# Optimization experiments

Hardware: AMD Instinct MI355X
Metric: run time of the kernel (lower is better)

Reference implementation:

```python
import jax, jax.numpy as jnp
import numpy as np

B, N, V, E, T = 32, 256, 16, 1024, 5
MAX_N, ANNO, ND, VD, A_ACT = 256, 18, 64, 64, 3


def position_encoding_init(n_position, emb_dim):
    pe = np.array([[pos / np.power(10000, 2 * (j // 2) / emb_dim) for j in range(emb_dim)]
                   if pos != 0 else np.zeros(emb_dim) for pos in range(n_position)])
    pe[1:, 0::2] = np.sin(pe[1:, 0::2])
    pe[1:, 1::2] = np.cos(pe[1:, 1::2])
    return jnp.asarray(pe, jnp.float32)


def gru_cell(x, h, Wih, Whh, bih=None, bhh=None):
    # PyTorch GRUCell semantics. Wih: [3H, in], Whh: [3H, H]
    gi = x @ Wih.T + (bih if bih is not None else 0.0)
    gh = h @ Whh.T + (bhh if bhh is not None else 0.0)
    i_r, i_z, i_n = jnp.split(gi, 3, axis=1)
    h_r, h_z, h_n = jnp.split(gh, 3, axis=1)
    r = jax.nn.sigmoid(i_r + h_r)
    z = jax.nn.sigmoid(i_z + h_z)
    n = jnp.tanh(i_n + r * h_n)
    return (1.0 - z) * n + z * h


def setup_inputs() -> dict:
    key = jax.random.key(0)
    ks = jax.random.split(key, 20)
    dec_in = E + ND + 2 * VD
    inp = {
        "annotation": jax.random.normal(ks[0], (B, N, ANNO), jnp.float32),
        "A_out": jax.random.bernoulli(ks[1], 0.05, (B, N, N)).astype(jnp.float32),
        "A_in": jax.random.bernoulli(ks[2], 0.05, (B, N, N)).astype(jnp.float32),
        "from_node": jax.random.randint(ks[3], (B,), 0, MAX_N),
        "vnf_now": jax.random.uniform(ks[4], (B, V), jnp.float32),
        "vnf_all": jax.random.uniform(ks[5], (B, V), jnp.float32),
        "mask": jax.random.randint(ks[6], (B * N,), 0, 2),
        "anno_W": jax.random.normal(ks[7], (ANNO, E), jnp.float32),
        "gru_Wih": jax.random.normal(ks[8], (3 * E, 2 * E), jnp.float32) / np.sqrt(2 * E),
        "gru_Whh": jax.random.normal(ks[9], (3 * E, E), jnp.float32) / np.sqrt(E),
        "vnf_now_W": jax.random.normal(ks[10], (V, VD), jnp.float32),
        "vnf_all_W": jax.random.normal(ks[11], (V, VD), jnp.float32),
        "dgru_Wih": jax.random.normal(ks[12], (6 * E, dec_in), jnp.float32) / np.sqrt(dec_in),
        "dgru_Whh": jax.random.normal(ks[13], (6 * E, 2 * E), jnp.float32) / np.sqrt(2 * E),
        "dgru_bih": jax.random.normal(ks[14], (6 * E,), jnp.float32) * 0.01,
        "dgru_bhh": jax.random.normal(ks[15], (6 * E,), jnp.float32) * 0.01,
        "out_W1": jax.random.normal(ks[16], (E, 2 * E), jnp.float32) / np.sqrt(2 * E),
        "out_b1": jnp.zeros((E,), jnp.float32),
        "out_W2": jax.random.normal(ks[17], (A_ACT, E), jnp.float32) / np.sqrt(E),
        "out_b2": jnp.zeros((A_ACT,), jnp.float32),
        "pos_enc": position_encoding_init(MAX_N, ND),
    }
    return inp


def reference(annotation, A_out, A_in, from_node, vnf_now, vnf_all, mask,
              anno_W, gru_Wih, gru_Whh, vnf_now_W, vnf_all_W,
              dgru_Wih, dgru_Whh, dgru_bih, dgru_bhh,
              out_W1, out_b1, out_W2, out_b2, pos_enc):
    BN = B * N
    # ---- encoder (GG-NN): block-diagonal adjacency matmul == batched matmul ----
    h = annotation.reshape(BN, ANNO) @ anno_W  # [BN, E]

    def step(h, _):
        hb = h.reshape(B, N, E)
        a_out = jnp.einsum('bnm,bme->bne', A_out, hb).reshape(BN, E)
        a_in = jnp.einsum('bnm,bme->bne', A_in, hb).reshape(BN, E)
        a = jnp.concatenate([a_out, a_in], axis=1)  # [BN, 2E]
        return gru_cell(a, h, gru_Wih, gru_Whh), None

    enc_out, _ = jax.lax.scan(step, h, None, length=T)  # [BN, E]

    # ---- decoder step ----
    vn = (vnf_now @ vnf_now_W)[:, None, :]  # [B,1,VD] (repeat over N)
    va = (vnf_all @ vnf_all_W)[:, None, :]
    npos = pos_enc[from_node][:, None, :]   # [B,1,ND]
    vn = jnp.broadcast_to(vn, (B, N, VD)).reshape(BN, VD)
    va = jnp.broadcast_to(va, (B, N, VD)).reshape(BN, VD)
    npos = jnp.broadcast_to(npos, (B, N, ND)).reshape(BN, ND)

    concat_input = jnp.concatenate([enc_out, npos, va, vn], axis=1)
    h0 = jnp.zeros((BN, 2 * E), jnp.float32)
    hidden = gru_cell(concat_input, h0, dgru_Wih, dgru_Whh, dgru_bih, dgru_bhh)

    mid = jax.nn.relu(hidden @ out_W1.T + out_b1)
    output = (mid @ out_W2.T + out_b2).reshape(B, N, A_ACT)

    max_v = jnp.max(output, axis=(1, 2), keepdims=True)  # [B,1,1]
    output = output - (max_v + 1.0)
    mask_f = jnp.where(mask == 1, 1.0, 1e10).astype(jnp.float32).reshape(B, N, 1)
    output = mask_f * output + 1.0

    node_logits = output[:, :, 0]            # [B, N]
    vnf_logits = output[:, :, 1:]            # [B, N, 2]
    return node_logits, vnf_logits, hidden
```

## Files before the change

kernel.cpp:

```cpp
#include <hip/hip_runtime.h>
#include <hip/hip_bf16.h>
#include <math.h>

#define B_ 32
#define N_ 256
#define E_ 1024
#define BN_ 8192

typedef __hip_bfloat16 bf16;
typedef __bf16 bf8v __attribute__((ext_vector_type(8)));
typedef float  f4v  __attribute__((ext_vector_type(4)));

__device__ __forceinline__ float b2f(bf16 v) {
    unsigned short u = *(unsigned short*)&v;
    return __uint_as_float(((unsigned)u) << 16);
}
__device__ __forceinline__ unsigned short f2bu(float f) {
    bf16 h = __float2bfloat16(f);
    return *(unsigned short*)&h;
}
__device__ __forceinline__ float4 load4bf(const bf16* p) {
    ushort4 u = *(const ushort4*)p;
    return make_float4(__uint_as_float((unsigned)u.x << 16),
                       __uint_as_float((unsigned)u.y << 16),
                       __uint_as_float((unsigned)u.z << 16),
                       __uint_as_float((unsigned)u.w << 16));
}
__device__ __forceinline__ void store4bf(bf16* p, float a, float b, float c, float d) {
    ushort4 u = make_ushort4(f2bu(a), f2bu(b), f2bu(c), f2bu(d));
    *(ushort4*)p = u;
}
__device__ __forceinline__ float safe_sigm(float x) {
    x = fminf(fmaxf(x, -40.0f), 40.0f);
    return 1.0f / (1.0f + expf(-x));
}
__device__ __forceinline__ float safe_tanh(float x) {
    x = fminf(fmaxf(x, -15.0f), 15.0f);
    float t = expf(2.0f * x);
    return (t - 1.0f) / (t + 1.0f);
}
__device__ __forceinline__ void glds16(const bf16* g, bf16* l) {
    __builtin_amdgcn_global_load_lds(
        (__attribute__((address_space(1))) const void*)g,
        (__attribute__((address_space(3))) void*)l, 16, 0, 0);
}

#define MFMA16(d, a, b) d = __builtin_amdgcn_mfma_f32_16x16x32_bf16(a, b, d, 0, 0, 0)

__global__ __launch_bounds__(256)
void w2bf_kernel(const float* __restrict__ src, bf16* __restrict__ dst, int n4)
{
    int i = blockIdx.x * 256 + threadIdx.x;
    if (i < n4) {
        float4 v = ((const float4*)src)[i];
        store4bf(dst + (size_t)i * 4, v.x, v.y, v.z, v.w);
    }
}

__global__ __launch_bounds__(256)
void wgpack_kernel(const float* __restrict__ Wih, const float* __restrict__ Whh,
                   bf16* __restrict__ Wg)
{
    const int wr = blockIdx.x;
    const int e16 = wr / 48, rem = wr % 48;
    const int gate = rem >> 4, eL = rem & 15;
    const int e = e16 * 16 + eL;
    const float* s1 = Wih + (size_t)(gate * 1024 + e) * 2048;
    const float* s2 = Whh + (size_t)(gate * 1024 + e) * 1024;
    bf16* d = Wg + (size_t)wr * 3072;
    const int k0 = threadIdx.x * 4;
#pragma unroll
    for (int rep = 0; rep < 2; ++rep) {
        int k = k0 + rep * 1024;
        float4 v = *(const float4*)(s1 + k);
        store4bf(d + k, v.x, v.y, v.z, v.w);
    }
    {
        float4 v = *(const float4*)(s2 + k0);
        store4bf(d + 2048 + k0, v.x, v.y, v.z, v.w);
    }
}

__global__ __launch_bounds__(256)
void dgpack_kernel(const float* __restrict__ Wih, bf16* __restrict__ Wg)
{
    const int wr = blockIdx.x;
    const int e16 = wr / 48, rem = wr % 48;
    const int gate = rem >> 4, eL = rem & 15;
    const int e = e16 * 16 + eL;
    const float* s = Wih + (size_t)(gate * 2048 + e) * 1216;
    bf16* d = Wg + (size_t)wr * 1216;
    for (int k4 = threadIdx.x; k4 < 304; k4 += 256) {
        float4 v = *(const float4*)(s + k4 * 4);
        store4bf(d + k4 * 4, v.x, v.y, v.z, v.w);
    }
}

__global__ __launch_bounds__(256)
void anno_kernel(const float* __restrict__ anno, const float* __restrict__ W,
                 float* __restrict__ H)
{
    __shared__ float s[18];
    int row = blockIdx.x;
    if (threadIdx.x < 18) s[threadIdx.x] = anno[row * 18 + threadIdx.x];
    __syncthreads();
    for (int j = threadIdx.x; j < 1024; j += 256) {
        float acc = 0.0f;
#pragma unroll
        for (int k = 0; k < 18; ++k) acc = fmaf(s[k], W[k * 1024 + j], acc);
        H[(size_t)row * 1024 + j] = acc;
    }
}

__global__ __launch_bounds__(256)
void bmm_kernel(const float* __restrict__ Aout, const float* __restrict__ Ain,
                const float* __restrict__ H, bf16* __restrict__ Abuf)
{
    __shared__ float As[16][68];
    __shared__ float Bs[16][68];
    const int z = blockIdx.z;
    const int b = z >> 1, which = z & 1;
    const float* Amat = (which ? Ain : Aout) + (size_t)b * N_ * N_;
    const float* Bmat = H + (size_t)b * N_ * E_;
    const int t = threadIdx.x;
    const int tx = t & 15, ty = t >> 4;
    const int bm = blockIdx.x * 64;
    const int bn = blockIdx.y * 64;
    const int ar = t >> 2, ak = (t & 3) << 2;
    const int kr = t >> 4, kn = (t & 15) << 2;
    float acc[4][4] = {};
    for (int k0 = 0; k0 < N_; k0 += 16) {
        float4 av = *(const float4*)(Amat + (size_t)(bm + ar) * N_ + k0 + ak);
        As[ak + 0][ar] = av.x; As[ak + 1][ar] = av.y;
        As[ak + 2][ar] = av.z; As[ak + 3][ar] = av.w;
        float4 bv = *(const float4*)(Bmat + (size_t)(k0 + kr) * E_ + bn + kn);
        *(float4*)&Bs[kr][kn] = bv;
        __syncthreads();
#pragma unroll
        for (int kk = 0; kk < 16; ++kk) {
            float4 a4 = *(const float4*)&As[kk][ty << 2];
            float4 b4 = *(const float4*)&Bs[kk][tx << 2];
            float am[4] = {a4.x, a4.y, a4.z, a4.w};
            float bb[4] = {b4.x, b4.y, b4.z, b4.w};
#pragma unroll
            for (int i = 0; i < 4; ++i)
#pragma unroll
                for (int j = 0; j < 4; ++j)
                    acc[i][j] = fmaf(am[i], bb[j], acc[i][j]);
        }
        __syncthreads();
    }
#pragma unroll
    for (int i = 0; i < 4; ++i) {
        int row = b * N_ + bm + (ty << 2) + i;
        int col = which * 1024 + bn + (tx << 2);
        store4bf(&Abuf[(size_t)row * 2048 + col], acc[i][0], acc[i][1], acc[i][2], acc[i][3]);
    }
}

__global__ __launch_bounds__(256)
void htrans_kernel(const float* __restrict__ H, bf16* __restrict__ HbT)
{
    __shared__ float s[64][65];
    const int b = blockIdx.z;
    const int e0 = blockIdx.x * 64;
    const int n0 = blockIdx.y * 64;
    const float* Hb = H + (size_t)b * N_ * E_;
    bf16* Tb = HbT + (size_t)b * E_ * N_;
    const int t = threadIdx.x;
    const int tr = t >> 4, tc = (t & 15) << 2;
#pragma unroll
    for (int i = 0; i < 4; ++i) {
        float4 v = *(const float4*)(Hb + (size_t)(n0 + tr + i * 16) * E_ + e0 + tc);
        s[tr + i * 16][tc + 0] = v.x; s[tr + i * 16][tc + 1] = v.y;
        s[tr + i * 16][tc + 2] = v.z; s[tr + i * 16][tc + 3] = v.w;
    }
    __syncthreads();
#pragma unroll
    for (int i = 0; i < 4; ++i) {
        int e = tr + i * 16;
        store4bf(Tb + (size_t)(e0 + e) * N_ + n0 + tc,
                 s[tc + 0][e], s[tc + 1][e], s[tc + 2][e], s[tc + 3][e]);
    }
}

__global__ __launch_bounds__(256)
void bmm_mfma_kernel(const bf16* __restrict__ Aoutb, const bf16* __restrict__ Ainb,
                     const bf16* __restrict__ HbT, bf16* __restrict__ Abuf)
{
    __shared__ bf16 As[64 * 32];
    __shared__ bf16 Bs[64 * 32];
    const int t = threadIdx.x;
    const int lane = t & 63, w = t >> 6;
    const int wm = (w >> 1) * 32, wn = (w & 1) * 32;
    const int z = blockIdx.z, b = z >> 1, which = z & 1;
    const int bm = blockIdx.x * 64, bn = blockIdx.y * 64;
    const int quad = lane >> 4, fr = lane & 15;
    const int srow = t >> 2, slot = t & 3;
    const int g = (slot + ((srow >> 1) & 3)) & 3;
    const int lds_off = srow * 32 + slot * 8;

    f4v acc[2][2];
#pragma unroll
    for (int i = 0; i < 2; ++i)
#pragma unroll
        for (int j = 0; j < 2; ++j) acc[i][j] = (f4v){0.f, 0.f, 0.f, 0.f};

    int aoff[2], boff[2];
#pragma unroll
    for (int i = 0; i < 2; ++i) {
        int arow = wm + 16 * i + fr;
        int s = (quad - ((arow >> 1) & 3)) & 3;
        aoff[i] = arow * 32 + s * 8;
    }
#pragma unroll
    for (int j = 0; j < 2; ++j) {
        int n = wn + 16 * j + fr;
        int s = (quad - ((n >> 1) & 3)) & 3;
        boff[j] = n * 32 + s * 8;
    }

    const bf16* Ap = (which ? Ainb : Aoutb) + (size_t)b * N_ * N_
                   + (size_t)(bm + srow) * N_ + g * 8;
    const bf16* Bp = HbT + (size_t)b * E_ * N_ + (size_t)(bn + srow) * N_ + g * 8;
    for (int k0 = 0; k0 < N_; k0 += 32) {
        float4 av = *(const float4*)(Ap + k0);
        float4 bv4 = *(const float4*)(Bp + k0);
        __syncthreads();
        *(float4*)(As + lds_off) = av;
        *(float4*)(Bs + lds_off) = bv4;
        __syncthreads();
        bf8v af0 = *(const bf8v*)(As + aoff[0]);
        bf8v af1 = *(const bf8v*)(As + aoff[1]);
#pragma unroll
        for (int j = 0; j < 2; ++j) {
            bf8v bv = *(const bf8v*)(Bs + boff[j]);
            MFMA16(acc[0][j], af0, bv);
            MFMA16(acc[1][j], af1, bv);
        }
    }
#pragma unroll
    for (int i = 0; i < 2; ++i)
#pragma unroll
        for (int j = 0; j < 2; ++j)
#pragma unroll
            for (int r = 0; r < 4; ++r) {
                int row = b * N_ + bm + wm + 16 * i + quad * 4 + r;
                int col = which * 1024 + bn + wn + 16 * j + fr;
                Abuf[(size_t)row * 2048 + col] = __float2bfloat16(acc[i][j][r]);
            }
}

__global__ __launch_bounds__(256, 2)
void enc_gru_kernel(const bf16* __restrict__ Aab, const bf16* __restrict__ Wg,
                    const float* __restrict__ Hcur, float* __restrict__ Hnext)
{
    __shared__ __align__(16) bf16 As[2 * 128 * 32];
    __shared__ __align__(16) bf16 Bs[2 * 192 * 32];
    const int t = threadIdx.x;
    const int lane = t & 63, w = t >> 6;
    const int wm = (w >> 1) * 64;
    const int wnH = (w & 1);
    const int bm = blockIdx.x * 128;
    const int bY = blockIdx.y;
    const int quad = lane >> 4, fr = lane & 15;

    f4v ar[2][4], az[2][4], ani[2][4], anh[2][4];
#pragma unroll
    for (int gq = 0; gq < 2; ++gq)
#pragma unroll
        for (int i = 0; i < 4; ++i) {
            ar[gq][i] = (f4v){0.f, 0.f, 0.f, 0.f};
            az[gq][i] = (f4v){0.f, 0.f, 0.f, 0.f};
            ani[gq][i] = (f4v){0.f, 0.f, 0.f, 0.f};
            anh[gq][i] = (f4v){0.f, 0.f, 0.f, 0.f};
        }

    int aoff[4];
#pragma unroll
    for (int i = 0; i < 4; ++i) {
        int row = wm + 16 * i + fr;
        int s = (quad - ((row >> 1) & 3)) & 3;
        aoff[i] = row * 32 + s * 8;
    }
    int boff[2][3];
#pragma unroll
    for (int gq = 0; gq < 2; ++gq)
#pragma unroll
        for (int gt = 0; gt < 3; ++gt) {
            int nb = wnH * 96 + gq * 48 + gt * 16 + fr;
            int s = (quad - ((nb >> 1) & 3)) & 3;
            boff[gq][gt] = nb * 32 + s * 8;
        }

    const int sr = lane >> 2, ss = lane & 3;
    const int lrA0 = w * 16 + sr;
    const int lrA1 = 64 + w * 16 + sr;
    const int gA0 = (ss + ((lrA0 >> 1) & 3)) & 3;
    const int gA1 = (ss + ((lrA1 >> 1) & 3)) & 3;
    const bf16* apA0 = Aab + (size_t)(bm + lrA0) * 2048 + gA0 * 8;
    const bf16* apA1 = Aab + (size_t)(bm + lrA1) * 2048 + gA1 * 8;
    const int lrB0 = w * 16 + sr, lrB1 = 64 + w * 16 + sr, lrB2 = 128 + w * 16 + sr;
    const int gB0 = (ss + ((lrB0 >> 1) & 3)) & 3;
    const int gB1 = (ss + ((lrB1 >> 1) & 3)) & 3;
    const int gB2 = (ss + ((lrB2 >> 1) & 3)) & 3;
    const bf16* bp0 = Wg + (size_t)(bY * 192 + lrB0) * 3072 + gB0 * 8;
    const bf16* bp1 = Wg + (size_t)(bY * 192 + lrB1) * 3072 + gB1 * 8;
    const bf16* bp2 = Wg + (size_t)(bY * 192 + lrB2) * 3072 + gB2 * 8;
    const int oA0 = (w * 16) * 32, oA1 = (64 + w * 16) * 32;
    const int oB0 = (w * 16) * 32, oB1 = (64 + w * 16) * 32, oB2 = (128 + w * 16) * 32;

#define ENC_STEP(Ab, Bb, AN) do {                                              \
    bf8v af0 = *(const bf8v*)((Ab) + aoff[0]);                                 \
    bf8v af1 = *(const bf8v*)((Ab) + aoff[1]);                                 \
    bf8v af2 = *(const bf8v*)((Ab) + aoff[2]);                                 \
    bf8v af3 = *(const bf8v*)((Ab) + aoff[3]);                                 \
    _Pragma("unroll")                                                          \
    for (int gq = 0; gq < 2; ++gq) {                                           \
        bf8v br_ = *(const bf8v*)((Bb) + boff[gq][0]);                         \
        bf8v bz_ = *(const bf8v*)((Bb) + boff[gq][1]);                         \
        bf8v bn_ = *(const bf8v*)((Bb) + boff[gq][2]);                         \
        MFMA16(ar[gq][0], af0, br_); MFMA16(ar[gq][1], af1, br_);              \
        MFMA16(ar[gq][2], af2, br_); MFMA16(ar[gq][3], af3, br_);              \
        MFMA16(az[gq][0], af0, bz_); MFMA16(az[gq][1], af1, bz_);              \
        MFMA16(az[gq][2], af2, bz_); MFMA16(az[gq][3], af3, bz_);              \
        MFMA16(AN[gq][0], af0, bn_); MFMA16(AN[gq][1], af1, bn_);              \
        MFMA16(AN[gq][2], af2, bn_); MFMA16(AN[gq][3], af3, bn_);              \
    }                                                                          \
} while (0)

    glds16(apA0, As + oA0);
    glds16(apA1, As + oA1);
    glds16(bp0, Bs + oB0);
    glds16(bp1, Bs + oB1);
    glds16(bp2, Bs + oB2);
    __syncthreads();
    int cur = 0;
    for (int k0 = 0; k0 < 2048; k0 += 32) {
        const int nb = cur ^ 1;
        if (k0 + 32 < 2048) {
            glds16(apA0 + k0 + 32, As + nb * 4096 + oA0);
            glds16(apA1 + k0 + 32, As + nb * 4096 + oA1);
            glds16(bp0 + k0 + 32, Bs + nb * 6144 + oB0);
            glds16(bp1 + k0 + 32, Bs + nb * 6144 + oB1);
            glds16(bp2 + k0 + 32, Bs + nb * 6144 + oB2);
        }
        const bf16* Ab = As + cur * 4096;
        const bf16* Bb = Bs + cur * 6144;
        ENC_STEP(Ab, Bb, ani);
        __syncthreads();
        cur = nb;
    }

    {
        const int tr = t >> 1;
        const int c0 = (t & 1) * 2;
        const int rr_ = (tr >> 1) & 3;
        const int s0 = (c0 - rr_) & 3;
        const int s1 = (c0 + 1 - rr_) & 3;
        const float* hp = Hcur + (size_t)(bm + tr) * 1024 + c0 * 8;
        for (int k0 = 2048; k0 < 3072; k0 += 32) {
            const int k2 = k0 - 2048;
            float4 f0 = *(const float4*)(hp + k2);
            float4 f1 = *(const float4*)(hp + k2 + 4);
            float4 f2 = *(const float4*)(hp + k2 + 8);
            float4 f3 = *(const float4*)(hp + k2 + 12);
            uint4 u0, u1;
            u0.x = (unsigned)f2bu(f0.x) | ((unsigned)f2bu(f0.y) << 16);
            u0.y = (unsigned)f2bu(f0.z) | ((unsigned)f2bu(f0.w) << 16);
            u0.z = (unsigned)f2bu(f1.x) | ((unsigned)f2bu(f1.y) << 16);
            u0.w = (unsigned)f2bu(f1.z) | ((unsigned)f2bu(f1.w) << 16);
            u1.x = (unsigned)f2bu(f2.x) | ((unsigned)f2bu(f2.y) << 16);
            u1.y = (unsigned)f2bu(f2.z) | ((unsigned)f2bu(f2.w) << 16);
            u1.z = (unsigned)f2bu(f3.x) | ((unsigned)f2bu(f3.y) << 16);
            u1.w = (unsigned)f2bu(f3.z) | ((unsigned)f2bu(f3.w) << 16);
            __syncthreads();
            *(uint4*)(As + tr * 32 + s0 * 8) = u0;
            *(uint4*)(As + tr * 32 + s1 * 8) = u1;
            glds16(bp0 + k0, Bs + oB0);
            glds16(bp1 + k0, Bs + oB1);
            glds16(bp2 + k0, Bs + oB2);
            __syncthreads();
            ENC_STEP(As, Bs, anh);
        }
    }

#pragma unroll
    for (int gq = 0; gq < 2; ++gq) {
        const int e = bY * 64 + wnH * 32 + gq * 16 + fr;
#pragma unroll
        for (int i = 0; i < 4; ++i) {
#pragma unroll
            for (int r = 0; r < 4; ++r) {
                const int row = bm + wm + 16 * i + quad * 4 + r;
                float hv = Hcur[(size_t)row * 1024 + e];
                float rg = safe_sigm(ar[gq][i][r]);
                float zg = safe_sigm(az[gq][i][r]);
                float ng = safe_tanh(ani[gq][i][r] + rg * anh[gq][i][r]);
                Hnext[(size_t)row * 1024 + e] = (1.0f - zg) * ng + zg * hv;
            }
        }
    }
#undef ENC_STEP
}

__global__ __launch_bounds__(256, 2)
void dec_gru_kernel(const bf16* __restrict__ Cc, const bf16* __restrict__ Wg,
                    const float* __restrict__ bih, const float* __restrict__ bhh,
                    float* __restrict__ hidden)
{
    __shared__ __align__(16) bf16 As[2 * 128 * 32];
    __shared__ __align__(16) bf16 Bs[2 * 192 * 32];
    const int t = threadIdx.x;
    const int lane = t & 63, w = t >> 6;
    const int wm = (w >> 1) * 64;
    const int wnH = (w & 1);
    const int bm = blockIdx.x * 128;
    const int bY = blockIdx.y;
    const int quad = lane >> 4, fr = lane & 15;

    f4v ag[3][2][4];
#pragma unroll
    for (int c = 0; c < 3; ++c)
#pragma unroll
        for (int gq = 0; gq < 2; ++gq)
#pragma unroll
            for (int i = 0; i < 4; ++i) ag[c][gq][i] = (f4v){0.f, 0.f, 0.f, 0.f};

    int aoff[4];
#pragma unroll
    for (int i = 0; i < 4; ++i) {
        int row = wm + 16 * i + fr;
        int s = (quad - ((row >> 1) & 3)) & 3;
        aoff[i] = row * 32 + s * 8;
    }
    int boff[2][3];
#pragma unroll
    for (int gq = 0; gq < 2; ++gq)
#pragma unroll
        for (int gt = 0; gt < 3; ++gt) {
            int nb = wnH * 96 + gq * 48 + gt * 16 + fr;
            int s = (quad - ((nb >> 1) & 3)) & 3;
            boff[gq][gt] = nb * 32 + s * 8;
        }

    const int sr = lane >> 2, ss = lane & 3;
    const int lrA0 = w * 16 + sr;
    const int lrA1 = 64 + w * 16 + sr;
    const int gA0 = (ss + ((lrA0 >> 1) & 3)) & 3;
    const int gA1 = (ss + ((lrA1 >> 1) & 3)) & 3;
    const bf16* apA0 = Cc + (size_t)(bm + lrA0) * 1216 + gA0 * 8;
    const bf16* apA1 = Cc + (size_t)(bm + lrA1) * 1216 + gA1 * 8;
    const int lrB0 = w * 16 + sr, lrB1 = 64 + w * 16 + sr, lrB2 = 128 + w * 16 + sr;
    const int gB0 = (ss + ((lrB0 >> 1) & 3)) & 3;
    const int gB1 = (ss + ((lrB1 >> 1) & 3)) & 3;
    const int gB2 = (ss + ((lrB2 >> 1) & 3)) & 3;
    const bf16* bp0 = Wg + (size_t)(bY * 192 + lrB0) * 1216 + gB0 * 8;
    const bf16* bp1 = Wg + (size_t)(bY * 192 + lrB1) * 1216 + gB1 * 8;
    const bf16* bp2 = Wg + (size_t)(bY * 192 + lrB2) * 1216 + gB2 * 8;
    const int oA0 = (w * 16) * 32, oA1 = (64 + w * 16) * 32;
    const int oB0 = (w * 16) * 32, oB1 = (64 + w * 16) * 32, oB2 = (128 + w * 16) * 32;

    glds16(apA0, As + oA0);
    glds16(apA1, As + oA1);
    glds16(bp0, Bs + oB0);
    glds16(bp1, Bs + oB1);
    glds16(bp2, Bs + oB2);
    __syncthreads();
    int cur = 0;
    for (int k0 = 0; k0 < 1216; k0 += 32) {
        const int nb = cur ^ 1;
        if (k0 + 32 < 1216) {
            glds16(apA0 + k0 + 32, As + nb * 4096 + oA0);
            glds16(apA1 + k0 + 32, As + nb * 4096 + oA1);
            glds16(bp0 + k0 + 32, Bs + nb * 6144 + oB0);
            glds16(bp1 + k0 + 32, Bs + nb * 6144 + oB1);
            glds16(bp2 + k0 + 32, Bs + nb * 6144 + oB2);
        }
        const bf16* Ab = As + cur * 4096;
        const bf16* Bb = Bs + cur * 6144;
        bf8v af0 = *(const bf8v*)(Ab + aoff[0]);
        bf8v af1 = *(const bf8v*)(Ab + aoff[1]);
        bf8v af2 = *(const bf8v*)(Ab + aoff[2]);
        bf8v af3 = *(const bf8v*)(Ab + aoff[3]);
#pragma unroll
        for (int gq = 0; gq < 2; ++gq) {
            bf8v br_ = *(const bf8v*)(Bb + boff[gq][0]);
            bf8v bz_ = *(const bf8v*)(Bb + boff[gq][1]);
            bf8v bn_ = *(const bf8v*)(Bb + boff[gq][2]);
            MFMA16(ag[0][gq][0], af0, br_); MFMA16(ag[0][gq][1], af1, br_);
            MFMA16(ag[0][gq][2], af2, br_); MFMA16(ag[0][gq][3], af3, br_);
            MFMA16(ag[1][gq][0], af0, bz_); MFMA16(ag[1][gq][1], af1, bz_);
            MFMA16(ag[1][gq][2], af2, bz_); MFMA16(ag[1][gq][3], af3, bz_);
            MFMA16(ag[2][gq][0], af0, bn_); MFMA16(ag[2][gq][1], af1, bn_);
            MFMA16(ag[2][gq][2], af2, bn_); MFMA16(ag[2][gq][3], af3, bn_);
        }
        __syncthreads();
        cur = nb;
    }

#pragma unroll
    for (int gq = 0; gq < 2; ++gq) {
        const int e = bY * 64 + wnH * 32 + gq * 16 + fr;
        const float br = bih[e] + bhh[e];
        const float bz = bih[2048 + e] + bhh[2048 + e];
        const float bni = bih[4096 + e];
        const float bnh = bhh[4096 + e];
#pragma unroll
        for (int i = 0; i < 4; ++i) {
#pragma unroll
            for (int r = 0; r < 4; ++r) {
                const int row = bm + wm + 16 * i + quad * 4 + r;
                float rr = safe_sigm(ag[0][gq][i][r] + br);
                float zz = safe_sigm(ag[1][gq][i][r] + bz);
                float nn = safe_tanh(ag[2][gq][i][r] + bni + rr * bnh);
                hidden[(size_t)row * 2048 + e] = (1.0f - zz) * nn;
            }
        }
    }
}

__global__ __launch_bounds__(128)
void vnva_kernel(const float* __restrict__ vnf_now, const float* __restrict__ vnf_all,
                 const float* __restrict__ Wn, const float* __restrict__ Wa,
                 float* __restrict__ vn, float* __restrict__ va)
{
    int b = blockIdx.x, t = threadIdx.x;
    if (t < 64) {
        float s = 0.f;
#pragma unroll
        for (int k = 0; k < 16; ++k) s = fmaf(vnf_now[b * 16 + k], Wn[k * 64 + t], s);
        vn[b * 64 + t] = s;
    } else {
        int d = t - 64;
        float s = 0.f;
#pragma unroll
        for (int k = 0; k < 16; ++k) s = fmaf(vnf_all[b * 16 + k], Wa[k * 64 + d], s);
        va[b * 64 + d] = s;
    }
}

__global__ __launch_bounds__(256)
void concat_kernel(const float* __restrict__ H, const float* __restrict__ pos_enc,
                   const int* __restrict__ from_node, const float* __restrict__ va,
                   const float* __restrict__ vn, bf16* __restrict__ Cc)
{
    int row = blockIdx.x;
    int b = row >> 8;
    int fn = from_node[b];
    bf16* dst = Cc + (size_t)row * 1216;
    for (int c = threadIdx.x; c < 1216; c += 256) {
        float v;
        if (c < 1024)      v = H[(size_t)row * 1024 + c];
        else if (c < 1088) v = pos_enc[fn * 64 + (c - 1024)];
        else if (c < 1152) v = va[b * 64 + (c - 1088)];
        else               v = vn[b * 64 + (c - 1152)];
        dst[c] = __float2bfloat16(v);
    }
}

__global__ __launch_bounds__(256)
void out1_mfma_kernel(const float* __restrict__ H, const bf16* __restrict__ W1b,
                      const float* __restrict__ bias, bf16* __restrict__ mid)
{
    __shared__ bf16 As[64 * 32];
    __shared__ bf16 Ws[256 * 32];
    const int t = threadIdx.x;
    const int lane = t & 63, w = t >> 6;
    const int bm = blockIdx.x * 64, bn = blockIdx.y * 256;
    const int quad = lane >> 4, fr = lane & 15;
    const int srow = t >> 2, slot = t & 3;
    const int g = (slot + ((srow >> 1) & 3)) & 3;
    const int lds_off = srow * 32 + slot * 8;

    f4v acc[4][4];
#pragma unroll
    for (int i = 0; i < 4; ++i)
#pragma unroll
        for (int j = 0; j < 4; ++j) acc[i][j] = (f4v){0.f, 0.f, 0.f, 0.f};

    int aoff[4], boff[4];
#pragma unroll
    for (int i = 0; i < 4; ++i) {
        int arow = 16 * i + fr;
        int s = (quad - ((arow >> 1) & 3)) & 3;
        aoff[i] = arow * 32 + s * 8;
    }
#pragma unroll
    for (int j = 0; j < 4; ++j) {
        int n = w * 64 + 16 * j + fr;
        int s = (quad - ((n >> 1) & 3)) & 3;
        boff[j] = n * 32 + s * 8;
    }

    const float* Hp = H + (size_t)(bm + srow) * 2048 + g * 8;
    const bf16* Wp0 = W1b + (size_t)(bn + srow) * 2048 + g * 8;
    const bf16* Wp1 = W1b + (size_t)(bn + srow + 64) * 2048 + g * 8;
    const bf16* Wp2 = W1b + (size_t)(bn + srow + 128) * 2048 + g * 8;
    const bf16* Wp3 = W1b + (size_t)(bn + srow + 192) * 2048 + g * 8;

    for (int k0 = 0; k0 < 2048; k0 += 32) {
        float4 h0 = *(const float4*)(Hp + k0);
        float4 h1 = *(const float4*)(Hp + k0 + 4);
        float4 w0 = *(const float4*)(Wp0 + k0);
        float4 w1 = *(const float4*)(Wp1 + k0);
        float4 w2 = *(const float4*)(Wp2 + k0);
        float4 w3 = *(const float4*)(Wp3 + k0);
        uint4 pk;
        pk.x = (unsigned)f2bu(h0.x) | ((unsigned)f2bu(h0.y) << 16);
        pk.y = (unsigned)f2bu(h0.z) | ((unsigned)f2bu(h0.w) << 16);
        pk.z = (unsigned)f2bu(h1.x) | ((unsigned)f2bu(h1.y) << 16);
        pk.w = (unsigned)f2bu(h1.z) | ((unsigned)f2bu(h1.w) << 16);
        __syncthreads();
        *(uint4*)(As + lds_off) = pk;
        *(float4*)(Ws + lds_off) = w0;
        *(float4*)(Ws + 2048 + lds_off) = w1;
        *(float4*)(Ws + 4096 + lds_off) = w2;
        *(float4*)(Ws + 6144 + lds_off) = w3;
        __syncthreads();
        bf8v af0 = *(const bf8v*)(As + aoff[0]);
        bf8v af1 = *(const bf8v*)(As + aoff[1]);
        bf8v af2 = *(const bf8v*)(As + aoff[2]);
        bf8v af3 = *(const bf8v*)(As + aoff[3]);
#pragma unroll
        for (int j = 0; j < 4; ++j) {
            bf8v bv = *(const bf8v*)(Ws + boff[j]);
            MFMA16(acc[0][j], af0, bv);
            MFMA16(acc[1][j], af1, bv);
            MFMA16(acc[2][j], af2, bv);
            MFMA16(acc[3][j], af3, bv);
        }
    }
#pragma unroll
    for (int j = 0; j < 4; ++j) {
        const int col = bn + w * 64 + 16 * j + fr;
        const float bb = bias[col];
#pragma unroll
        for (int i = 0; i < 4; ++i) {
#pragma unroll
            for (int r = 0; r < 4; ++r) {
                const int row = bm + 16 * i + quad * 4 + r;
                mid[(size_t)row * 1024 + col] = __float2bfloat16(fmaxf(acc[i][j][r] + bb, 0.0f));
            }
        }
    }
}

__global__ __launch_bounds__(64)
void out2_kernel(const bf16* __restrict__ mid, const float* __restrict__ W2,
                 const float* __restrict__ b2, float* __restrict__ outb)
{
    int row = blockIdx.x, t = threadIdx.x;
    float s0 = 0.f, s1 = 0.f, s2 = 0.f;
    for (int k = t; k < 1024; k += 64) {
        float m = b2f(mid[(size_t)row * 1024 + k]);
        s0 = fmaf(m, W2[k], s0);
        s1 = fmaf(m, W2[1024 + k], s1);
        s2 = fmaf(m, W2[2048 + k], s2);
    }
#pragma unroll
    for (int off = 32; off > 0; off >>= 1) {
        s0 += __shfl_down(s0, off, 64);
        s1 += __shfl_down(s1, off, 64);
        s2 += __shfl_down(s2, off, 64);
    }
    if (t == 0) {
        outb[row * 3 + 0] = s0 + b2[0];
        outb[row * 3 + 1] = s1 + b2[1];
        outb[row * 3 + 2] = s2 + b2[2];
    }
}

__global__ __launch_bounds__(64)
void max_kernel(const float* __restrict__ outb, float* __restrict__ maxb)
{
    int b = blockIdx.x, t = threadIdx.x;
    float m = -3.0e38f;
    for (int i = t; i < 768; i += 64) m = fmaxf(m, outb[b * 768 + i]);
#pragma unroll
    for (int off = 32; off > 0; off >>= 1) m = fmaxf(m, __shfl_down(m, off, 64));
    if (t == 0) maxb[b] = m;
}

__global__ __launch_bounds__(256)
void mask_kernel(const float* __restrict__ outb, const float* __restrict__ maxb,
                 const int* __restrict__ mask, float* __restrict__ out)
{
    int idx = blockIdx.x * 256 + threadIdx.x;
    if (idx >= BN_ * 3) return;
    int row = idx / 3, c = idx - row * 3;
    int b = row >> 8;
    float v = outb[idx] - (maxb[b] + 1.0f);
    float mf = (mask[row] == 1) ? 1.0f : 1e10f;
    v = mf * v + 1.0f;
    if (c == 0) out[row] = v;
    else        out[8192 + row * 2 + (c - 1)] = v;
}

extern "C" void kernel_launch(void* const* d_in, const int* in_sizes, int n_in,
                              void* d_out, int out_size, void* d_ws, size_t ws_size,
                              hipStream_t stream)
{
    const float* annotation = (const float*)d_in[0];
    const float* A_out      = (const float*)d_in[1];
    const float* A_in       = (const float*)d_in[2];
    const int*   from_node  = (const int*)d_in[3];
    const float* vnf_now    = (const float*)d_in[4];
    const float* vnf_all    = (const float*)d_in[5];
    const int*   mask       = (const int*)d_in[6];
    const float* anno_W     = (const float*)d_in[7];
    const float* gru_Wih    = (const float*)d_in[8];
    const float* gru_Whh    = (const float*)d_in[9];
    const float* vnf_now_W  = (const float*)d_in[10];
    const float* vnf_all_W  = (const float*)d_in[11];
    const float* dgru_Wih   = (const float*)d_in[12];
    const float* dgru_bih   = (const float*)d_in[14];
    const float* dgru_bhh   = (const float*)d_in[15];
    const float* out_W1     = (const float*)d_in[16];
    const float* out_b1     = (const float*)d_in[17];
    const float* out_W2     = (const float*)d_in[18];
    const float* out_b2     = (const float*)d_in[19];
    const float* pos_enc    = (const float*)d_in[20];
    float* out = (float*)d_out;

    bf16*  Abuf = (bf16*)d_ws;
    bf16*  Wenc = Abuf + (size_t)8192 * 2048;
    bf16*  Wg   = Wenc;
    bf16*  WgD  = Wenc;
    bf16*  W1b  = Wenc;
    float* fbuf = (float*)(Wenc + (size_t)9437184);
    float* vnb  = fbuf;
    float* vab  = vnb + 2048;
    float* outb = vab + 2048;
    float* maxb = outb + 24576;
    bf16*  Aoutb = (bf16*)(maxb + 32);
    bf16*  Ainb  = Aoutb + (size_t)32 * 256 * 256;
    bf16*  HbT   = Ainb + (size_t)32 * 256 * 256;

    const size_t NEED_FULL = (size_t)(16777216 + 9437184) * 2 + 28704 * 4
                           + (size_t)(4194304 + 8388608) * 2;
    const bool full = ws_size >= NEED_FULL;

    float* hidden = out + 24576;
    float* H0 = hidden;
    float* H1 = H0 + (size_t)8192 * 1024;
    bf16* Cc  = Abuf;
    bf16* mid = Abuf;

    wgpack_kernel<<<3072, 256, 0, stream>>>(gru_Wih, gru_Whh, Wg);
    if (full) {
        w2bf_kernel<<<2048, 256, 0, stream>>>(A_out, Aoutb, 32 * 256 * 256 / 4);
        w2bf_kernel<<<2048, 256, 0, stream>>>(A_in,  Ainb,  32 * 256 * 256 / 4);
    }

    anno_kernel<<<8192, 256, 0, stream>>>(annotation, anno_W, H0);

    const float* hc = H0;
    float* hn = H1;
    for (int s = 0; s < 5; ++s) {
        if (full) {
            htrans_kernel<<<dim3(16, 4, 32), 256, 0, stream>>>(hc, HbT);
            bmm_mfma_kernel<<<dim3(4, 16, 64), 256, 0, stream>>>(Aoutb, Ainb, HbT, Abuf);
        } else {
            bmm_kernel<<<dim3(4, 16, 64), 256, 0, stream>>>(A_out, A_in, hc, Abuf);
        }
        enc_gru_kernel<<<dim3(64, 16), 256, 0, stream>>>(Abuf, Wg, hc, hn);
        float* tmp = (float*)hc; hc = hn; hn = tmp;
    }

    vnva_kernel<<<32, 128, 0, stream>>>(vnf_now, vnf_all, vnf_now_W, vnf_all_W, vnb, vab);
    concat_kernel<<<8192, 256, 0, stream>>>(hc, pos_enc, from_node, vab, vnb, Cc);

    dgpack_kernel<<<6144, 256, 0, stream>>>(dgru_Wih, WgD);
    dec_gru_kernel<<<dim3(64, 32), 256, 0, stream>>>(Cc, WgD, dgru_bih, dgru_bhh, hidden);

    w2bf_kernel<<<2048, 256, 0, stream>>>(out_W1, W1b, 1024 * 2048 / 4);
    out1_mfma_kernel<<<dim3(128, 4), 256, 0, stream>>>(hidden, W1b, out_b1, mid);

    out2_kernel<<<8192, 64, 0, stream>>>(mid, out_W2, out_b2, outb);
    max_kernel<<<32, 64, 0, stream>>>(outb, maxb);
    mask_kernel<<<96, 256, 0, stream>>>(outb, maxb, mask, out);
}
```

Baseline: 1.668 ms.

## Store encoder hidden state in bf16 and pipeline GRU K-loop with async staging

The encoder hidden state H moves from fp32 to bf16 storage throughout: anno, htrans, bmm, enc_gru and concat. This halves hidden-state traffic and lets the Hcur part of the GRU GEMM be staged with async global-to-LDS loads instead of converting on the fly with extra barriers. The GRU K-loop becomes a deeper software pipeline that keeps two stages in flight, using explicit vmcnt waits and raw barriers. The risk is extra rounding error from carrying the recurrent state in bf16 across the five steps.

```diff
diff --git a/kernel.cpp b/kernel.cpp
--- a/kernel.cpp
+++ b/kernel.cpp
@@ -98,7 +98,7 @@
 
 __global__ __launch_bounds__(256)
 void anno_kernel(const float* __restrict__ anno, const float* __restrict__ W,
-                 float* __restrict__ H)
+                 bf16* __restrict__ Hb)
 {
     __shared__ float s[18];
     int row = blockIdx.x;
@@ -108,20 +108,20 @@
         float acc = 0.0f;
 #pragma unroll
         for (int k = 0; k < 18; ++k) acc = fmaf(s[k], W[k * 1024 + j], acc);
-        H[(size_t)row * 1024 + j] = acc;
+        Hb[(size_t)row * 1024 + j] = __float2bfloat16(acc);
     }
 }
 
 __global__ __launch_bounds__(256)
 void bmm_kernel(const float* __restrict__ Aout, const float* __restrict__ Ain,
-                const float* __restrict__ H, bf16* __restrict__ Abuf)
+                const bf16* __restrict__ H, bf16* __restrict__ Abuf)
 {
     __shared__ float As[16][68];
     __shared__ float Bs[16][68];
     const int z = blockIdx.z;
     const int b = z >> 1, which = z & 1;
     const float* Amat = (which ? Ain : Aout) + (size_t)b * N_ * N_;
-    const float* Bmat = H + (size_t)b * N_ * E_;
+    const bf16* Bmat = H + (size_t)b * N_ * E_;
     const int t = threadIdx.x;
     const int tx = t & 15, ty = t >> 4;
     const int bm = blockIdx.x * 64;
@@ -133,7 +133,7 @@
         float4 av = *(const float4*)(Amat + (size_t)(bm + ar) * N_ + k0 + ak);
         As[ak + 0][ar] = av.x; As[ak + 1][ar] = av.y;
         As[ak + 2][ar] = av.z; As[ak + 3][ar] = av.w;
-        float4 bv = *(const float4*)(Bmat + (size_t)(k0 + kr) * E_ + bn + kn);
+        float4 bv = load4bf(Bmat + (size_t)(k0 + kr) * E_ + bn + kn);
         *(float4*)&Bs[kr][kn] = bv;
         __syncthreads();
 #pragma unroll
@@ -159,19 +159,19 @@
 }
 
 __global__ __launch_bounds__(256)
-void htrans_kernel(const float* __restrict__ H, bf16* __restrict__ HbT)
+void htrans_kernel(const bf16* __restrict__ H, bf16* __restrict__ HbT)
 {
     __shared__ float s[64][65];
     const int b = blockIdx.z;
     const int e0 = blockIdx.x * 64;
     const int n0 = blockIdx.y * 64;
-    const float* Hb = H + (size_t)b * N_ * E_;
+    const bf16* Hb = H + (size_t)b * N_ * E_;
     bf16* Tb = HbT + (size_t)b * E_ * N_;
     const int t = threadIdx.x;
     const int tr = t >> 4, tc = (t & 15) << 2;
 #pragma unroll
     for (int i = 0; i < 4; ++i) {
-        float4 v = *(const float4*)(Hb + (size_t)(n0 + tr + i * 16) * E_ + e0 + tc);
+        float4 v = load4bf(Hb + (size_t)(n0 + tr + i * 16) * E_ + e0 + tc);
         s[tr + i * 16][tc + 0] = v.x; s[tr + i * 16][tc + 1] = v.y;
         s[tr + i * 16][tc + 2] = v.z; s[tr + i * 16][tc + 3] = v.w;
     }
@@ -253,7 +253,7 @@
 
 __global__ __launch_bounds__(256, 2)
 void enc_gru_kernel(const bf16* __restrict__ Aab, const bf16* __restrict__ Wg,
-                    const float* __restrict__ Hcur, float* __restrict__ Hnext)
+                    const bf16* __restrict__ Hcur, bf16* __restrict__ Hnext)
 {
     __shared__ __align__(16) bf16 As[2 * 128 * 32];
     __shared__ __align__(16) bf16 Bs[2 * 192 * 32];
@@ -300,6 +300,8 @@
     const int gA1 = (ss + ((lrA1 >> 1) & 3)) & 3;
     const bf16* apA0 = Aab + (size_t)(bm + lrA0) * 2048 + gA0 * 8;
     const bf16* apA1 = Aab + (size_t)(bm + lrA1) * 2048 + gA1 * 8;
+    const bf16* hpA0 = Hcur + (size_t)(bm + lrA0) * 1024 + gA0 * 8;
+    const bf16* hpA1 = Hcur + (size_t)(bm + lrA1) * 1024 + gA1 * 8;
     const int lrB0 = w * 16 + sr, lrB1 = 64 + w * 16 + sr, lrB2 = 128 + w * 16 + sr;
     const int gB0 = (ss + ((lrB0 >> 1) & 3)) & 3;
     const int gB1 = (ss + ((lrB1 >> 1) & 3)) & 3;
@@ -309,6 +311,17 @@
     const bf16* bp2 = Wg + (size_t)(bY * 192 + lrB2) * 3072 + gB2 * 8;
     const int oA0 = (w * 16) * 32, oA1 = (64 + w * 16) * 32;
     const int oB0 = (w * 16) * 32, oB1 = (64 + w * 16) * 32, oB2 = (128 + w * 16) * 32;
+
+#define ENC_STAGE(K, BUF) do {                                                 \
+    const int k_ = (K);                                                        \
+    const bf16* a0_ = (k_ < 2048) ? apA0 + k_ : hpA0 + (k_ - 2048);            \
+    const bf16* a1_ = (k_ < 2048) ? apA1 + k_ : hpA1 + (k_ - 2048);            \
+    glds16(a0_, As + (BUF) * 4096 + oA0);                                      \
+    glds16(a1_, As + (BUF) * 4096 + oA1);                                      \
+    glds16(bp0 + k_, Bs + (BUF) * 6144 + oB0);                                 \
+    glds16(bp1 + k_, Bs + (BUF) * 6144 + oB1);                                 \
+    glds16(bp2 + k_, Bs + (BUF) * 6144 + oB2);                                 \
+} while (0)
 
 #define ENC_STEP(Ab, Bb, AN) do {                                              \
     bf8v af0 = *(const bf8v*)((Ab) + aoff[0]);                                 \
@@ -329,61 +342,30 @@
     }                                                                          \
 } while (0)
 
-    glds16(apA0, As + oA0);
-    glds16(apA1, As + oA1);
-    glds16(bp0, Bs + oB0);
-    glds16(bp1, Bs + oB1);
-    glds16(bp2, Bs + oB2);
-    __syncthreads();
+    ENC_STAGE(0, 0);
+    ENC_STAGE(32, 1);
     int cur = 0;
+#pragma unroll 2
     for (int k0 = 0; k0 < 2048; k0 += 32) {
-        const int nb = cur ^ 1;
-        if (k0 + 32 < 2048) {
-            glds16(apA0 + k0 + 32, As + nb * 4096 + oA0);
-            glds16(apA1 + k0 + 32, As + nb * 4096 + oA1);
-            glds16(bp0 + k0 + 32, Bs + nb * 6144 + oB0);
-            glds16(bp1 + k0 + 32, Bs + nb * 6144 + oB1);
-            glds16(bp2 + k0 + 32, Bs + nb * 6144 + oB2);
-        }
-        const bf16* Ab = As + cur * 4096;
-        const bf16* Bb = Bs + cur * 6144;
-        ENC_STEP(Ab, Bb, ani);
-        __syncthreads();
-        cur = nb;
-    }
-
-    {
-        const int tr = t >> 1;
-        const int c0 = (t & 1) * 2;
-        const int rr_ = (tr >> 1) & 3;
-        const int s0 = (c0 - rr_) & 3;
-        const int s1 = (c0 + 1 - rr_) & 3;
-        const float* hp = Hcur + (size_t)(bm + tr) * 1024 + c0 * 8;
-        for (int k0 = 2048; k0 < 3072; k0 += 32) {
-            const int k2 = k0 - 2048;
-            float4 f0 = *(const float4*)(hp + k2);
-            float4 f1 = *(const float4*)(hp + k2 + 4);
-            float4 f2 = *(const float4*)(hp + k2 + 8);
-            float4 f3 = *(const float4*)(hp + k2 + 12);
-            uint4 u0, u1;
-            u0.x = (unsigned)f2bu(f0.x) | ((unsigned)f2bu(f0.y) << 16);
-            u0.y = (unsigned)f2bu(f0.z) | ((unsigned)f2bu(f0.w) << 16);
-            u0.z = (unsigned)f2bu(f1.x) | ((unsigned)f2bu(f1.y) << 16);
-            u0.w = (unsigned)f2bu(f1.z) | ((unsigned)f2bu(f1.w) << 16);
-            u1.x = (unsigned)f2bu(f2.x) | ((unsigned)f2bu(f2.y) << 16);
-            u1.y = (unsigned)f2bu(f2.z) | ((unsigned)f2bu(f2.w) << 16);
-            u1.z = (unsigned)f2bu(f3.x) | ((unsigned)f2bu(f3.y) << 16);
-            u1.w = (unsigned)f2bu(f3.z) | ((unsigned)f2bu(f3.w) << 16);
-            __syncthreads();
-            *(uint4*)(As + tr * 32 + s0 * 8) = u0;
-            *(uint4*)(As + tr * 32 + s1 * 8) = u1;
-            glds16(bp0 + k0, Bs + oB0);
-            glds16(bp1 + k0, Bs + oB1);
-            glds16(bp2 + k0, Bs + oB2);
-            __syncthreads();
-            ENC_STEP(As, Bs, anh);
-        }
-    }
+        asm volatile("s_waitcnt vmcnt(5)" ::: "memory");
+        __builtin_amdgcn_s_barrier();
+        ENC_STEP(As + cur * 4096, Bs + cur * 6144, ani);
+        __builtin_amdgcn_s_barrier();
+        ENC_STAGE(k0 + 64, cur);
+        cur ^= 1;
+    }
+#pragma unroll 2
+    for (int k0 = 2048; k0 < 3040; k0 += 32) {
+        asm volatile("s_waitcnt vmcnt(5)" ::: "memory");
+        __builtin_amdgcn_s_barrier();
+        ENC_STEP(As + cur * 4096, Bs + cur * 6144, anh);
+        __builtin_amdgcn_s_barrier();
+        if (k0 + 64 < 3072) ENC_STAGE(k0 + 64, cur);
+        cur ^= 1;
+    }
+    asm volatile("s_waitcnt vmcnt(0)" ::: "memory");
+    __builtin_amdgcn_s_barrier();
+    ENC_STEP(As + cur * 4096, Bs + cur * 6144, anh);
 
 #pragma unroll
     for (int gq = 0; gq < 2; ++gq) {
@@ -393,15 +375,17 @@
 #pragma unroll
             for (int r = 0; r < 4; ++r) {
                 const int row = bm + wm + 16 * i + quad * 4 + r;
-                float hv = Hcur[(size_t)row * 1024 + e];
+                float hv = b2f(Hcur[(size_t)row * 1024 + e]);
                 float rg = safe_sigm(ar[gq][i][r]);
                 float zg = safe_sigm(az[gq][i][r]);
                 float ng = safe_tanh(ani[gq][i][r] + rg * anh[gq][i][r]);
-                Hnext[(size_t)row * 1024 + e] = (1.0f - zg) * ng + zg * hv;
+                Hnext[(size_t)row * 1024 + e] =
+                    __float2bfloat16((1.0f - zg) * ng + zg * hv);
             }
         }
     }
 #undef ENC_STEP
+#undef ENC_STAGE
 }
 
 __global__ __launch_bounds__(256, 2)
@@ -541,21 +525,30 @@
 }
 
 __global__ __launch_bounds__(256)
-void concat_kernel(const float* __restrict__ H, const float* __restrict__ pos_enc,
+void concat_kernel(const bf16* __restrict__ H, const float* __restrict__ pos_enc,
                    const int* __restrict__ from_node, const float* __restrict__ va,
                    const float* __restrict__ vn, bf16* __restrict__ Cc)
 {
     int row = blockIdx.x;
     int b = row >> 8;
     int fn = from_node[b];
+    const bf16* hsrc = H + (size_t)row * 1024;
     bf16* dst = Cc + (size_t)row * 1216;
-    for (int c = threadIdx.x; c < 1216; c += 256) {
-        float v;
-        if (c < 1024)      v = H[(size_t)row * 1024 + c];
-        else if (c < 1088) v = pos_enc[fn * 64 + (c - 1024)];
-        else if (c < 1152) v = va[b * 64 + (c - 1088)];
-        else               v = vn[b * 64 + (c - 1152)];
-        dst[c] = __float2bfloat16(v);
+    for (int c8 = threadIdx.x; c8 < 152; c8 += 256) {
+        int c = c8 * 8;
+        if (c < 1024) {
+            *(uint4*)(dst + c) = *(const uint4*)(hsrc + c);
+        } else {
+#pragma unroll
+            for (int j = 0; j < 8; ++j) {
+                int col = c + j;
+                float v;
+                if (col < 1088)      v = pos_enc[fn * 64 + (col - 1024)];
+                else if (col < 1152) v = va[b * 64 + (col - 1088)];
+                else                 v = vn[b * 64 + (col - 1152)];
+                dst[col] = __float2bfloat16(v);
+            }
+        }
     }
 }
 
@@ -742,8 +735,8 @@
     const bool full = ws_size >= NEED_FULL;
 
     float* hidden = out + 24576;
-    float* H0 = hidden;
-    float* H1 = H0 + (size_t)8192 * 1024;
+    bf16* Hb0 = (bf16*)hidden;
+    bf16* Hb1 = Hb0 + (size_t)8192 * 1024;
     bf16* Cc  = Abuf;
     bf16* mid = Abuf;
 
@@ -753,10 +746,10 @@
         w2bf_kernel<<<2048, 256, 0, stream>>>(A_in,  Ainb,  32 * 256 * 256 / 4);
     }
 
-    anno_kernel<<<8192, 256, 0, stream>>>(annotation, anno_W, H0);
-
-    const float* hc = H0;
-    float* hn = H1;
+    anno_kernel<<<8192, 256, 0, stream>>>(annotation, anno_W, Hb0);
+
+    const bf16* hc = Hb0;
+    bf16* hn = Hb1;
     for (int s = 0; s < 5; ++s) {
         if (full) {
             htrans_kernel<<<dim3(16, 4, 32), 256, 0, stream>>>(hc, HbT);
@@ -765,7 +758,7 @@
             bmm_kernel<<<dim3(4, 16, 64), 256, 0, stream>>>(A_out, A_in, hc, Abuf);
         }
         enc_gru_kernel<<<dim3(64, 16), 256, 0, stream>>>(Abuf, Wg, hc, hn);
-        float* tmp = (float*)hc; hc = hn; hn = tmp;
+        bf16* tmp = (bf16*)hc; hc = hn; hn = tmp;
     }
 
     vnva_kernel<<<32, 128, 0, stream>>>(vnf_now, vnf_all, vnf_now_W, vnf_all_W, vnb, vab);
```

After: 1.512 ms. 1.1x faster.
